# Kernel optimization log

Hardware: AMD Instinct MI355X
Metric: run time of the kernel (lower is better)

The kernel has to match this reference:

```python
import jax, jax.numpy as jnp
import numpy as np
import math

D_MODEL = 1024
NUM_HEADS = 16
HEAD_DIM = D_MODEL // NUM_HEADS
THETA = 10000.0
B, S = 2, 2048


def apply_rope(x, pos, theta=THETA):
    # x: [..., S, D]; pos: [S] int. Rotates consecutive (even, odd) pairs.
    d = x.shape[-1]
    inv_freq = theta ** (-jnp.arange(0, d, 2, dtype=jnp.float32) / d)  # [d/2]
    ang = pos.astype(jnp.float32)[:, None] * inv_freq[None, :]          # [S, d/2]
    cos, sin = jnp.cos(ang), jnp.sin(ang)
    xe = x[..., 0::2]
    xo = x[..., 1::2]
    re = xe * cos - xo * sin
    ro = xe * sin + xo * cos
    return jnp.stack([re, ro], axis=-1).reshape(x.shape)


def setup_inputs() -> dict:
    key = jax.random.key(0)
    ks = jax.random.split(key, 5)
    scale = 1.0 / math.sqrt(D_MODEL)
    return {
        "in_features": jax.random.normal(ks[0], (B, S, D_MODEL), dtype=jnp.float32),
        "token_positions": jnp.arange(S, dtype=jnp.int32),
        "wq": jax.random.normal(ks[1], (D_MODEL, D_MODEL), dtype=jnp.float32) * scale,
        "wk": jax.random.normal(ks[2], (D_MODEL, D_MODEL), dtype=jnp.float32) * scale,
        "wv": jax.random.normal(ks[3], (D_MODEL, D_MODEL), dtype=jnp.float32) * scale,
        "wo": jax.random.normal(ks[4], (D_MODEL, D_MODEL), dtype=jnp.float32) * scale,
    }


def reference(in_features, token_positions, wq, wk, wv, wo):
    x = in_features
    b, s, d = x.shape
    # Linear: y = x @ W.T  (weight stored as [out, in])
    def split_heads(y):
        return y.reshape(b, s, NUM_HEADS, HEAD_DIM).transpose(0, 2, 1, 3)  # [B,H,S,Dh]
    Q = split_heads(x @ wq.T)
    K = split_heads(x @ wk.T)
    V = split_heads(x @ wv.T)
    Q = apply_rope(Q, token_positions)
    K = apply_rope(K, token_positions)
    scores = jnp.einsum('bhqd,bhkd->bhqk', Q, K) / math.sqrt(HEAD_DIM)
    causal = jnp.tril(jnp.ones((s, s), dtype=bool))
    scores = jnp.where(causal, scores, -jnp.inf)
    weights = jax.nn.softmax(scores, axis=-1)
    out = jnp.einsum('bhqk,bhkd->bhqd', weights, V)  # [B,H,S,Dh]
    out = out.transpose(0, 2, 1, 3).reshape(b, s, d)
    return out @ wo.T
```

## Files before the change

kernel.cpp:

```cpp
#include <hip/hip_runtime.h>
#include <hip/hip_bf16.h>

typedef __bf16 bf16_t;
typedef __bf16 bf16x8 __attribute__((ext_vector_type(8)));
typedef __bf16 bf16x4 __attribute__((ext_vector_type(4)));
typedef float  f32x4  __attribute__((ext_vector_type(4)));
typedef float  f32x16 __attribute__((ext_vector_type(16)));
typedef unsigned int u32;
typedef unsigned int u32x2v __attribute__((ext_vector_type(2)));
typedef unsigned int u32x4v __attribute__((ext_vector_type(4)));

#define D_MODEL   1024
#define NQKV      3072
#define NUM_HEADS 16
#define HEAD_DIM  64
#define SEQ       2048
#define BATCH     2
#define NTOK      4096
#define SM_SCALE_LOG2E 0.18033688011112042f
#define NEG_BIG  (-3.0e38f)

__device__ __forceinline__ int swz128(int row, int bytecol) {
  return row*128 + ((((bytecol>>4) ^ (row&7))<<4) | (bytecol & 15));
}

__device__ __forceinline__ void gload16(const void* g, void* l) {
  __builtin_amdgcn_global_load_lds((const __attribute__((address_space(1))) u32*)g,
                                   (__attribute__((address_space(3))) u32*)l, 16, 0, 0);
}

__device__ __forceinline__ u32 cvtpk_bf16(float a, float b) {
  u32 r;
  asm("v_cvt_pk_bf16_f32 %0, %1, %2" : "=v"(r) : "v"(a), "v"(b));
  return r;
}

__device__ __forceinline__ void plswap(u32 &a, u32 &b) {
#if __has_builtin(__builtin_amdgcn_permlane32_swap)
  u32x2v r = __builtin_amdgcn_permlane32_swap(a, b, false, false);
  a = r[0]; b = r[1];
#else
  u32 xa = __shfl_xor((unsigned)a, 32, 64);
  u32 xb = __shfl_xor((unsigned)b, 32, 64);
  bool hi = (threadIdx.x & 32) != 0;
  a = hi ? xb : a;
  b = hi ? b : xa;
#endif
}

__device__ const unsigned char slot_order96[96] = {
  30,31,88,90,92,93,94,95,
  28,29,80,82,84,85,86,87,89,91,
  26,27,72,74,76,77,78,79,81,83,
  24,25,64,66,68,69,70,71,73,75,
  22,23,56,58,60,61,62,63,65,67,
  20,21,48,50,52,53,54,55,57,59,
  18,19,40,42,44,45,46,47,49,51,
  16,17,32,34,36,37,38,39,41,43,
  14,15,33,35,
  12,13, 10,11, 8,9, 6,7, 4,5, 2,3, 0,1
};

__global__ void cvt_x(const float* __restrict__ in, bf16_t* __restrict__ out) {
  int i = (blockIdx.x*256 + threadIdx.x)*4;
  float4 v = *reinterpret_cast<const float4*>(in + i);
  bf16x4 o; o[0]=(bf16_t)v.x; o[1]=(bf16_t)v.y; o[2]=(bf16_t)v.z; o[3]=(bf16_t)v.w;
  *reinterpret_cast<bf16x4*>(out + i) = o;
}

__global__ void cvt_w(const float* __restrict__ wq, const float* __restrict__ wk,
                      const float* __restrict__ wv, const float* __restrict__ wo,
                      bf16_t* __restrict__ wqkv, bf16_t* __restrict__ wob) {
  const int NW = D_MODEL*D_MODEL;
  int i = (blockIdx.x*256 + threadIdx.x)*4;
  float4 v;
  if      (i <   NW) v = *reinterpret_cast<const float4*>(wq + i);
  else if (i < 2*NW) v = *reinterpret_cast<const float4*>(wk + i - NW);
  else if (i < 3*NW) v = *reinterpret_cast<const float4*>(wv + i - 2*NW);
  else               v = *reinterpret_cast<const float4*>(wo + i - 3*NW);
  bf16x4 o; o[0]=(bf16_t)v.x; o[1]=(bf16_t)v.y; o[2]=(bf16_t)v.z; o[3]=(bf16_t)v.w;
  bf16_t* dst = (i < 3*NW) ? (wqkv + i) : (wob + i - 3*NW);
  *reinterpret_cast<bf16x4*>(dst) = o;
}

__global__ void rope_qk(bf16_t* __restrict__ QKV, const int* __restrict__ pos) {
  int i = blockIdx.x*256 + threadIdx.x;
  int j = i & 31;
  int hp = (i >> 5) & 15;
  int t  = i >> 9;
  float ang = (float)pos[t & (SEQ-1)] * exp2f(-(float)j * (13.287712379549449f/32.0f));
  float sv, cv; sincosf(ang, &sv, &cv);
  size_t base = (size_t)t*NQKV + hp*64 + 2*j;
  float xe = (float)QKV[base], xo = (float)QKV[base+1];
  QKV[base]   = (bf16_t)((xe*cv - xo*sv)*SM_SCALE_LOG2E);
  QKV[base+1] = (bf16_t)((xe*sv + xo*cv)*SM_SCALE_LOG2E);
  xe = (float)QKV[base+1024]; xo = (float)QKV[base+1025];
  QKV[base+1024] = (bf16_t)(xe*cv - xo*sv);
  QKV[base+1025] = (bf16_t)(xe*sv + xo*cv);
}

template<typename OutT, bool QKV>
__global__ __launch_bounds__(256, 1) void gemm8(const bf16_t* __restrict__ A,
                                                const bf16_t* __restrict__ B,
                                                OutT* __restrict__ C,
                                                bf16_t* __restrict__ Vt,
                                                int M, int N, int K) {
  __shared__ __align__(16) char lds[4][32768];
  int tid = threadIdx.x;
  int n0 = blockIdx.x*128, m0 = blockIdx.y*128;
  int wid = tid>>6, lane = tid&63;
  int wr = wid>>1, wc = wid&1;
  int lr = lane&15, lg = lane>>4;

  const int nT = K >> 6;

  int srow = tid >> 3;
  int sc8  = (tid & 7) ^ (srow & 7);
  const bf16_t* ga = A + (size_t)(m0 + srow)*K + sc8*8;
  const bf16_t* gb = B + (size_t)(n0 + srow)*K + sc8*8;

  f32x4 acc[4][4];
  #pragma unroll
  for (int a=0;a<4;a++)
    #pragma unroll
    for (int b=0;b<4;b++) acc[a][b] = (f32x4){0.f,0.f,0.f,0.f};

  auto stage = [&](int t) {
    char* s = lds[t&3];
    int k0 = t << 6;
    #pragma unroll
    for (int g=0; g<4; g++)
      gload16(ga + (size_t)(g*32)*K + k0, s + g*4096 + tid*16);
    #pragma unroll
    for (int g=0; g<4; g++)
      gload16(gb + (size_t)(g*32)*K + k0, s + 16384 + g*4096 + tid*16);
  };

  stage(0);
  if (nT > 1) stage(1);
  asm volatile("s_waitcnt vmcnt(8)" ::: "memory");
  __builtin_amdgcn_sched_barrier(0);
  __builtin_amdgcn_s_barrier();

  for (int t = 0; t < nT; ++t) {
    char* sA = lds[t&3];
    char* sB = sA + 16384;

    bf16x8 bq[4][2], aq[2][2];
    #pragma unroll
    for (int ni=0; ni<4; ni++)
      #pragma unroll
      for (int ks=0; ks<2; ks++)
        bq[ni][ks] = *reinterpret_cast<const bf16x8*>(sB + swz128(wc*64+ni*16+lr, ks*64+lg*16));
    #pragma unroll
    for (int mi=0; mi<2; mi++)
      #pragma unroll
      for (int ks=0; ks<2; ks++)
        aq[mi][ks] = *reinterpret_cast<const bf16x8*>(sA + swz128(wr*64+mi*16+lr, ks*64+lg*16));
    if (t + 2 < nT) stage(t + 2);
    asm volatile("s_waitcnt lgkmcnt(0)" ::: "memory");
    __builtin_amdgcn_sched_barrier(0);
    __builtin_amdgcn_s_setprio(1);
    #pragma unroll
    for (int mi=0; mi<2; mi++)
      #pragma unroll
      for (int ni=0; ni<4; ni++)
        #pragma unroll
        for (int ks=0; ks<2; ks++)
          acc[mi][ni] = __builtin_amdgcn_mfma_f32_16x16x32_bf16(aq[mi][ks], bq[ni][ks], acc[mi][ni], 0, 0, 0);
    __builtin_amdgcn_s_setprio(0);
    __builtin_amdgcn_s_barrier();

    bf16x8 aq2[2][2];
    #pragma unroll
    for (int mi=0; mi<2; mi++)
      #pragma unroll
      for (int ks=0; ks<2; ks++)
        aq2[mi][ks] = *reinterpret_cast<const bf16x8*>(sA + swz128(wr*64+(mi+2)*16+lr, ks*64+lg*16));
    asm volatile("s_waitcnt lgkmcnt(0)" ::: "memory");
    __builtin_amdgcn_sched_barrier(0);
    __builtin_amdgcn_s_setprio(1);
    #pragma unroll
    for (int mi=0; mi<2; mi++)
      #pragma unroll
      for (int ni=0; ni<4; ni++)
        #pragma unroll
        for (int ks=0; ks<2; ks++)
          acc[mi+2][ni] = __builtin_amdgcn_mfma_f32_16x16x32_bf16(aq2[mi][ks], bq[ni][ks], acc[mi+2][ni], 0, 0, 0);
    __builtin_amdgcn_s_setprio(0);
    if (t + 2 < nT)      { asm volatile("s_waitcnt vmcnt(8)" ::: "memory"); }
    else if (t + 1 < nT) { asm volatile("s_waitcnt vmcnt(0)" ::: "memory"); }
    __builtin_amdgcn_sched_barrier(0);
    __builtin_amdgcn_s_barrier();
  }

  if (!QKV || n0 < 2*D_MODEL) {
    #pragma unroll
    for (int mi=0;mi<4;mi++)
      #pragma unroll
      for (int ni=0;ni<4;ni++)
        #pragma unroll
        for (int r=0;r<4;r++) {
          int m = m0 + wr*64 + mi*16 + lg*4 + r;
          int n = n0 + wc*64 + ni*16 + lr;
          C[(size_t)m*N + n] = (OutT)acc[mi][ni][r];
        }
  } else {
    #pragma unroll
    for (int mi=0;mi<4;mi++)
      #pragma unroll
      for (int ni=0;ni<4;ni++)
        #pragma unroll
        for (int r=0;r<4;r++) {
          int m = m0 + wr*64 + mi*16 + lg*4 + r;
          int nl = n0 + wc*64 + ni*16 + lr - 2*D_MODEL;
          int h = nl >> 6, d = nl & 63;
          int bb = m >> 11, s = m & (SEQ-1);
          Vt[(((size_t)(bb*16 + h)*64 + d) << 11) + s] = (bf16_t)acc[mi][ni][r];
        }
  }
}

__global__ __launch_bounds__(64, 2) void attn9(const bf16_t* __restrict__ QKV,
                                               const bf16_t* __restrict__ Vt,
                                               bf16_t* __restrict__ pO,
                                               float2* __restrict__ pML) {
  __shared__ __align__(16) char sK[64*128];
  __shared__ __align__(16) char sV[64*128];

  int bh = blockIdx.x;
  int b = bh >> 4, h = bh & 15;
  int lane = threadIdx.x & 63;
  int q32 = lane & 31, hi = lane >> 5;
  int rsub = lane >> 3, sg = (lane & 7) ^ rsub;

  int s = slot_order96[blockIdx.y];
  int qw, t0, t1;
  if (s < 32) { qw = s; t0 = 0; t1 = (s >> 1) + 1; }
  else {
    int e = s - 32;
    qw = 32 + (e >> 1);
    int nt = (qw >> 1) + 1, h0 = (nt + 1) >> 1;
    t0 = (e & 1) ? h0 : 0;
    t1 = (e & 1) ? nt : h0;
  }
  int qt   = qw >> 1;
  int slot = bh*96 + s;
  int qg   = qw*32 + q32;

  bf16x8 qf[4];
  const bf16_t* qrow = QKV + (size_t)(b*SEQ + qw*32 + q32)*NQKV + h*64 + hi*8;
  #pragma unroll
  for (int d=0; d<4; d++) qf[d] = *reinterpret_cast<const bf16x8*>(qrow + d*16);

  const bf16_t* kgb = QKV + D_MODEL + ((size_t)(b*SEQ) + rsub)*NQKV + h*64 + sg*8;
  const bf16_t* vgb = Vt + (size_t)bh*64*SEQ + (size_t)rsub*SEQ + sg*8;

  auto stageK = [&](int t) {
    const bf16_t* src = kgb + (size_t)t*64*NQKV;
    #pragma unroll
    for (int c=0;c<8;c++)
      gload16(src + (size_t)(8*c)*NQKV, sK + c*1024 + lane*16);
  };
  auto stageV = [&](int t) {
    const bf16_t* src = vgb + t*64;
    #pragma unroll
    for (int c=0;c<8;c++)
      gload16(src + (size_t)(8*c)*SEQ, sV + c*1024 + lane*16);
  };

  f32x16 O0 = (f32x16)0.0f, O1 = (f32x16)0.0f;
  float mrun = NEG_BIG, lrun = 0.f;

  stageK(t0); stageV(t0);
  asm volatile("s_waitcnt vmcnt(0)" ::: "memory");
  __builtin_amdgcn_sched_barrier(0);

  for (int ti = t0; ti < t1; ++ti) {
    bf16x8 k0f[4], k1f[4], v0f[4], v1f[4];
    #pragma unroll
    for (int ds=0; ds<4; ds++) {
      k0f[ds] = *reinterpret_cast<const bf16x8*>(sK + swz128(q32,    ds*32 + hi*16));
      k1f[ds] = *reinterpret_cast<const bf16x8*>(sK + swz128(32+q32, ds*32 + hi*16));
      v0f[ds] = *reinterpret_cast<const bf16x8*>(sV + swz128(q32,    ds*32 + hi*16));
      v1f[ds] = *reinterpret_cast<const bf16x8*>(sV + swz128(32+q32, ds*32 + hi*16));
    }
    asm volatile("s_waitcnt lgkmcnt(0)" ::: "memory");
    __builtin_amdgcn_sched_barrier(0);
    if (ti + 1 < t1) { stageK(ti + 1); stageV(ti + 1); }

    f32x16 p0 = (f32x16)0.0f, p1 = (f32x16)0.0f;
    __builtin_amdgcn_s_setprio(1);
    #pragma unroll
    for (int ds=0; ds<4; ds++) {
      p0 = __builtin_amdgcn_mfma_f32_32x32x16_bf16(k0f[ds], qf[ds], p0, 0, 0, 0);
      p1 = __builtin_amdgcn_mfma_f32_32x32x16_bf16(k1f[ds], qf[ds], p1, 0, 0, 0);
    }
    __builtin_amdgcn_s_setprio(0);

    if (ti == qt) {
      #pragma unroll
      for (int r=0; r<16; r++) {
        int kg = ti*64 + (r&3) + 8*(r>>2) + 4*hi;
        if (kg      > qg) p0[r] = NEG_BIG;
        if (kg + 32 > qg) p1[r] = NEG_BIG;
      }
    }

    float mx[8];
    #pragma unroll
    for (int r=0;r<8;r++) mx[r] = fmaxf(fmaxf(p0[r],p0[r+8]), fmaxf(p1[r],p1[r+8]));
    #pragma unroll
    for (int st=4; st>0; st>>=1)
      #pragma unroll
      for (int r=0;r<st;r++) mx[r] = fmaxf(mx[r], mx[r+st]);
    float mt   = fmaxf(mx[0], __shfl_xor(mx[0], 32, 64));
    float mnew = fmaxf(mrun, mt);
    float alpha = exp2f(mrun - mnew);
    #pragma unroll
    for (int r=0; r<16; r++) {
      p0[r] = exp2f(p0[r] - mnew);
      p1[r] = exp2f(p1[r] - mnew);
    }
    float sx[8];
    #pragma unroll
    for (int r=0;r<8;r++) sx[r] = (p0[r]+p0[r+8]) + (p1[r]+p1[r+8]);
    #pragma unroll
    for (int st=4; st>0; st>>=1)
      #pragma unroll
      for (int r=0;r<st;r++) sx[r] += sx[r+st];
    float stot = sx[0] + __shfl_xor(sx[0], 32, 64);
    lrun = lrun*alpha + stot;
    mrun = mnew;
    O0 *= alpha; O1 *= alpha;

    u32 pk0[8], pk1[8];
    #pragma unroll
    for (int i2=0; i2<8; i2++) {
      pk0[i2] = cvtpk_bf16(p0[2*i2], p0[2*i2+1]);
      pk1[i2] = cvtpk_bf16(p1[2*i2], p1[2*i2+1]);
    }
    plswap(pk0[0], pk0[2]); plswap(pk0[1], pk0[3]);
    plswap(pk0[4], pk0[6]); plswap(pk0[5], pk0[7]);
    plswap(pk1[0], pk1[2]); plswap(pk1[1], pk1[3]);
    plswap(pk1[4], pk1[6]); plswap(pk1[5], pk1[7]);

    bf16x8 pa[4];
    pa[0] = __builtin_bit_cast(bf16x8, (u32x4v){pk0[0],pk0[1],pk0[2],pk0[3]});
    pa[1] = __builtin_bit_cast(bf16x8, (u32x4v){pk0[4],pk0[5],pk0[6],pk0[7]});
    pa[2] = __builtin_bit_cast(bf16x8, (u32x4v){pk1[0],pk1[1],pk1[2],pk1[3]});
    pa[3] = __builtin_bit_cast(bf16x8, (u32x4v){pk1[4],pk1[5],pk1[6],pk1[7]});

    __builtin_amdgcn_s_setprio(1);
    #pragma unroll
    for (int ks=0; ks<4; ks++) {
      O0 = __builtin_amdgcn_mfma_f32_32x32x16_bf16(v0f[ks], pa[ks], O0, 0, 0, 0);
      O1 = __builtin_amdgcn_mfma_f32_32x32x16_bf16(v1f[ks], pa[ks], O1, 0, 0, 0);
    }
    __builtin_amdgcn_s_setprio(0);

    if (ti + 1 < t1) {
      asm volatile("s_waitcnt vmcnt(0)" ::: "memory");
      __builtin_amdgcn_sched_barrier(0);
    }
  }

  bf16_t* prow = pO + ((size_t)slot*2048 + q32*64);
  #pragma unroll
  for (int rg=0; rg<4; rg++) {
    int d0 = 8*rg + 4*hi;
    u32 a0 = cvtpk_bf16(O0[4*rg],   O0[4*rg+1]);
    u32 a1 = cvtpk_bf16(O0[4*rg+2], O0[4*rg+3]);
    *reinterpret_cast<u32x2v*>(prow + d0) = (u32x2v){a0, a1};
    u32 b0 = cvtpk_bf16(O1[4*rg],   O1[4*rg+1]);
    u32 b1 = cvtpk_bf16(O1[4*rg+2], O1[4*rg+3]);
    *reinterpret_cast<u32x2v*>(prow + 32 + d0) = (u32x2v){b0, b1};
  }
  if (hi == 0)
    pML[slot*32 + q32] = make_float2(mrun, lrun);
}

__global__ __launch_bounds__(128) void combine(const bf16_t* __restrict__ pO,
                                               const float2* __restrict__ pML,
                                               bf16_t* __restrict__ Of) {
  int qw = blockIdx.x, bh = blockIdx.y;
  int b = bh >> 4, h = bh & 15;
  int t = threadIdx.x;
  int q = t >> 2, d0 = (t & 3) * 16;
  bf16x8 r0, r1;
  if (qw < 32) {
    int slot = bh*96 + qw;
    float2 ml = pML[slot*32 + q];
    float inv = 1.0f / ml.y;
    const bf16x8* src = reinterpret_cast<const bf16x8*>(pO + (size_t)slot*2048 + q*64 + d0);
    bf16x8 o0 = src[0], o1 = src[1];
    #pragma unroll
    for (int i=0;i<8;i++) {
      r0[i] = (bf16_t)((float)o0[i]*inv);
      r1[i] = (bf16_t)((float)o1[i]*inv);
    }
  } else {
    int s0 = bh*96 + 32 + (qw-32)*2;
    float2 mlA = pML[s0*32 + q];
    float2 mlB = pML[(s0+1)*32 + q];
    float m  = fmaxf(mlA.x, mlB.x);
    float a0 = exp2f(mlA.x - m), a1 = exp2f(mlB.x - m);
    float inv = 1.0f / (a0*mlA.y + a1*mlB.y);
    a0 *= inv; a1 *= inv;
    const bf16x8* sA = reinterpret_cast<const bf16x8*>(pO + (size_t)s0*2048 + q*64 + d0);
    const bf16x8* sB = reinterpret_cast<const bf16x8*>(pO + (size_t)(s0+1)*2048 + q*64 + d0);
    bf16x8 oa0 = sA[0], oa1 = sA[1], ob0 = sB[0], ob1 = sB[1];
    #pragma unroll
    for (int i=0;i<8;i++) {
      r0[i] = (bf16_t)(a0*(float)oa0[i] + a1*(float)ob0[i]);
      r1[i] = (bf16_t)(a0*(float)oa1[i] + a1*(float)ob1[i]);
    }
  }
  bf16x8* dst = reinterpret_cast<bf16x8*>(Of + ((size_t)(b*SEQ) + qw*32 + q)*D_MODEL + h*64 + d0);
  dst[0] = r0; dst[1] = r1;
}

extern "C" void kernel_launch(void* const* d_in, const int* in_sizes, int n_in,
                              void* d_out, int out_size, void* d_ws, size_t ws_size,
                              hipStream_t stream) {
  const float* x   = (const float*)d_in[0];
  const int*   pos = (const int*)  d_in[1];
  const float* wq  = (const float*)d_in[2];
  const float* wk  = (const float*)d_in[3];
  const float* wv  = (const float*)d_in[4];
  const float* wo  = (const float*)d_in[5];
  float* out = (float*)d_out;

  char* ws = (char*)d_ws;
  bf16_t* xb   = (bf16_t*)(ws);
  bf16_t* wqkv = (bf16_t*)(ws + ( 8u<<20));
  bf16_t* wob  = (bf16_t*)(ws + (14u<<20));
  bf16_t* QKV  = (bf16_t*)(ws + (16u<<20));
  bf16_t* Vtb  = (bf16_t*)(ws + (40u<<20));
  bf16_t* pO   = (bf16_t*)(ws);
  float2* pML  = (float2*)(ws + (13u<<20));
  bf16_t* Of   = (bf16_t*)(ws + (40u<<20));

  cvt_x<<<NTOK*D_MODEL/1024, 256, 0, stream>>>(x, xb);
  cvt_w<<<4*D_MODEL*D_MODEL/1024, 256, 0, stream>>>(wq, wk, wv, wo, wqkv, wob);

  dim3 gqkv(NQKV/128, NTOK/128);
  gemm8<bf16_t, true><<<gqkv, 256, 0, stream>>>(xb, wqkv, QKV, Vtb, NTOK, NQKV, D_MODEL);

  rope_qk<<<NTOK*NUM_HEADS*32/256, 256, 0, stream>>>(QKV, pos);

  dim3 gattn(32, 96);
  attn9<<<gattn, 64, 0, stream>>>(QKV, Vtb, pO, pML);

  dim3 gcomb(64, 32);
  combine<<<gcomb, 128, 0, stream>>>(pO, pML, Of);

  dim3 gout(D_MODEL/128, NTOK/128);
  gemm8<float, false><<<gout, 256, 0, stream>>>(Of, wob, out, nullptr, NTOK, D_MODEL, D_MODEL);
}
```

Before: 131.3 us.

## Load V fragments directly from global, add lazy softmax rescale, raise occupancy

The attention kernel stops staging the transposed V tile through shared memory and reads V fragments straight from global memory into registers. This halves LDS use per block, and launch bounds rise from 2 to 3 waves per SIMD. The online softmax now rescales only when some lane's row max grows by more than 8 (in log2 units) over the running max, which skips the exp and multiply of the O accumulators on most tiles. The trade-off is that V global loads are no longer prefetched a tile ahead, so their latency is exposed. Raising the launch bound may also limit registers enough to cause spills.

```diff
diff --git a/kernel.cpp b/kernel.cpp
--- a/kernel.cpp
+++ b/kernel.cpp
@@ -221,12 +221,11 @@
   }
 }
 
-__global__ __launch_bounds__(64, 2) void attn9(const bf16_t* __restrict__ QKV,
-                                               const bf16_t* __restrict__ Vt,
-                                               bf16_t* __restrict__ pO,
-                                               float2* __restrict__ pML) {
+__global__ __launch_bounds__(64, 3) void attn10(const bf16_t* __restrict__ QKV,
+                                                const bf16_t* __restrict__ Vt,
+                                                bf16_t* __restrict__ pO,
+                                                float2* __restrict__ pML) {
   __shared__ __align__(16) char sK[64*128];
-  __shared__ __align__(16) char sV[64*128];
 
   int bh = blockIdx.x;
   int b = bh >> 4, h = bh & 15;
@@ -254,7 +253,8 @@
   for (int d=0; d<4; d++) qf[d] = *reinterpret_cast<const bf16x8*>(qrow + d*16);
 
   const bf16_t* kgb = QKV + D_MODEL + ((size_t)(b*SEQ) + rsub)*NQKV + h*64 + sg*8;
-  const bf16_t* vgb = Vt + (size_t)bh*64*SEQ + (size_t)rsub*SEQ + sg*8;
+  const bf16_t* vg0 = Vt + (size_t)bh*64*SEQ + (size_t)q32*SEQ + hi*8;
+  const bf16_t* vg1 = vg0 + (size_t)32*SEQ;
 
   auto stageK = [&](int t) {
     const bf16_t* src = kgb + (size_t)t*64*NQKV;
@@ -262,32 +262,30 @@
     for (int c=0;c<8;c++)
       gload16(src + (size_t)(8*c)*NQKV, sK + c*1024 + lane*16);
   };
-  auto stageV = [&](int t) {
-    const bf16_t* src = vgb + t*64;
-    #pragma unroll
-    for (int c=0;c<8;c++)
-      gload16(src + (size_t)(8*c)*SEQ, sV + c*1024 + lane*16);
-  };
 
   f32x16 O0 = (f32x16)0.0f, O1 = (f32x16)0.0f;
   float mrun = NEG_BIG, lrun = 0.f;
 
-  stageK(t0); stageV(t0);
+  stageK(t0);
   asm volatile("s_waitcnt vmcnt(0)" ::: "memory");
   __builtin_amdgcn_sched_barrier(0);
 
   for (int ti = t0; ti < t1; ++ti) {
-    bf16x8 k0f[4], k1f[4], v0f[4], v1f[4];
+    bf16x8 k0f[4], k1f[4];
     #pragma unroll
     for (int ds=0; ds<4; ds++) {
       k0f[ds] = *reinterpret_cast<const bf16x8*>(sK + swz128(q32,    ds*32 + hi*16));
       k1f[ds] = *reinterpret_cast<const bf16x8*>(sK + swz128(32+q32, ds*32 + hi*16));
-      v0f[ds] = *reinterpret_cast<const bf16x8*>(sV + swz128(q32,    ds*32 + hi*16));
-      v1f[ds] = *reinterpret_cast<const bf16x8*>(sV + swz128(32+q32, ds*32 + hi*16));
+    }
+    bf16x8 v0f[4], v1f[4];
+    #pragma unroll
+    for (int ks=0; ks<4; ks++) {
+      v0f[ks] = *reinterpret_cast<const bf16x8*>(vg0 + ti*64 + ks*16);
+      v1f[ks] = *reinterpret_cast<const bf16x8*>(vg1 + ti*64 + ks*16);
     }
     asm volatile("s_waitcnt lgkmcnt(0)" ::: "memory");
     __builtin_amdgcn_sched_barrier(0);
-    if (ti + 1 < t1) { stageK(ti + 1); stageV(ti + 1); }
+    if (ti + 1 < t1) stageK(ti + 1);
 
     f32x16 p0 = (f32x16)0.0f, p1 = (f32x16)0.0f;
     __builtin_amdgcn_s_setprio(1);
@@ -314,13 +312,19 @@
     for (int st=4; st>0; st>>=1)
       #pragma unroll
       for (int r=0;r<st;r++) mx[r] = fmaxf(mx[r], mx[r+st]);
-    float mt   = fmaxf(mx[0], __shfl_xor(mx[0], 32, 64));
-    float mnew = fmaxf(mrun, mt);
-    float alpha = exp2f(mrun - mnew);
+    float mt = fmaxf(mx[0], __shfl_xor(mx[0], 32, 64));
+
+    if (!__all(mt <= mrun + 8.0f)) {
+      float mnew  = fmaxf(mrun, mt);
+      float alpha = exp2f(mrun - mnew);
+      lrun *= alpha;
+      O0 *= alpha; O1 *= alpha;
+      mrun = mnew;
+    }
     #pragma unroll
     for (int r=0; r<16; r++) {
-      p0[r] = exp2f(p0[r] - mnew);
-      p1[r] = exp2f(p1[r] - mnew);
+      p0[r] = exp2f(p0[r] - mrun);
+      p1[r] = exp2f(p1[r] - mrun);
     }
     float sx[8];
     #pragma unroll
@@ -329,10 +333,7 @@
     for (int st=4; st>0; st>>=1)
       #pragma unroll
       for (int r=0;r<st;r++) sx[r] += sx[r+st];
-    float stot = sx[0] + __shfl_xor(sx[0], 32, 64);
-    lrun = lrun*alpha + stot;
-    mrun = mnew;
-    O0 *= alpha; O1 *= alpha;
+    lrun += sx[0] + __shfl_xor(sx[0], 32, 64);
 
     u32 pk0[8], pk1[8];
     #pragma unroll
@@ -450,7 +451,7 @@
   rope_qk<<<NTOK*NUM_HEADS*32/256, 256, 0, stream>>>(QKV, pos);
 
   dim3 gattn(32, 96);
-  attn9<<<gattn, 64, 0, stream>>>(QKV, Vtb, pO, pML);
+  attn10<<<gattn, 64, 0, stream>>>(QKV, Vtb, pO, pML);
 
   dim3 gcomb(64, 32);
   combine<<<gcomb, 128, 0, stream>>>(pO, pML, Of);
```

Result: slower. 136.9 us (+4.3%).

## Fuse RoPE into QKV GEMM epilogue and merge conversion kernels

Applied to the files above, without the earlier changes.

Removes the standalone rope_qk kernel by applying rotary embedding and the Q softmax scale inside the QKV GEMM epilogue. Adjacent even/odd columns are paired with a lane shuffle, and the angle comes from a fast __sincosf. The separate x and weight fp32-to-bf16 conversion kernels are also merged into one launch. This removes a read-modify-write pass over Q/K and a kernel launch, at the cost of more epilogue work and lower sin/cos accuracy at large angles.

```diff
diff --git a/kernel.cpp b/kernel.cpp
--- a/kernel.cpp
+++ b/kernel.cpp
@@ -18,6 +18,7 @@
 #define BATCH     2
 #define NTOK      4096
 #define SM_SCALE_LOG2E 0.18033688011112042f
+#define LOG2_THETA 13.287712379549449f
 #define NEG_BIG  (-3.0e38f)
 
 __device__ __forceinline__ int swz128(int row, int bytecol) {
@@ -61,42 +62,25 @@
   12,13, 10,11, 8,9, 6,7, 4,5, 2,3, 0,1
 };
 
-__global__ void cvt_x(const float* __restrict__ in, bf16_t* __restrict__ out) {
-  int i = (blockIdx.x*256 + threadIdx.x)*4;
-  float4 v = *reinterpret_cast<const float4*>(in + i);
-  bf16x4 o; o[0]=(bf16_t)v.x; o[1]=(bf16_t)v.y; o[2]=(bf16_t)v.z; o[3]=(bf16_t)v.w;
-  *reinterpret_cast<bf16x4*>(out + i) = o;
-}
-
-__global__ void cvt_w(const float* __restrict__ wq, const float* __restrict__ wk,
-                      const float* __restrict__ wv, const float* __restrict__ wo,
-                      bf16_t* __restrict__ wqkv, bf16_t* __restrict__ wob) {
+__global__ void cvt_all(const float* __restrict__ x,  const float* __restrict__ wq,
+                        const float* __restrict__ wk, const float* __restrict__ wv,
+                        const float* __restrict__ wo,
+                        bf16_t* __restrict__ xb, bf16_t* __restrict__ wqkv,
+                        bf16_t* __restrict__ wob) {
+  const int NX = NTOK*D_MODEL;
   const int NW = D_MODEL*D_MODEL;
   int i = (blockIdx.x*256 + threadIdx.x)*4;
-  float4 v;
-  if      (i <   NW) v = *reinterpret_cast<const float4*>(wq + i);
-  else if (i < 2*NW) v = *reinterpret_cast<const float4*>(wk + i - NW);
-  else if (i < 3*NW) v = *reinterpret_cast<const float4*>(wv + i - 2*NW);
-  else               v = *reinterpret_cast<const float4*>(wo + i - 3*NW);
+  float4 v; bf16_t* dst;
+  if (i < NX) { v = *reinterpret_cast<const float4*>(x + i); dst = xb + i; }
+  else {
+    int k = i - NX;
+    if      (k <   NW) { v = *reinterpret_cast<const float4*>(wq + k);        dst = wqkv + k; }
+    else if (k < 2*NW) { v = *reinterpret_cast<const float4*>(wk + k -   NW); dst = wqkv + k; }
+    else if (k < 3*NW) { v = *reinterpret_cast<const float4*>(wv + k - 2*NW); dst = wqkv + k; }
+    else               { v = *reinterpret_cast<const float4*>(wo + k - 3*NW); dst = wob + k - 3*NW; }
+  }
   bf16x4 o; o[0]=(bf16_t)v.x; o[1]=(bf16_t)v.y; o[2]=(bf16_t)v.z; o[3]=(bf16_t)v.w;
-  bf16_t* dst = (i < 3*NW) ? (wqkv + i) : (wob + i - 3*NW);
   *reinterpret_cast<bf16x4*>(dst) = o;
-}
-
-__global__ void rope_qk(bf16_t* __restrict__ QKV, const int* __restrict__ pos) {
-  int i = blockIdx.x*256 + threadIdx.x;
-  int j = i & 31;
-  int hp = (i >> 5) & 15;
-  int t  = i >> 9;
-  float ang = (float)pos[t & (SEQ-1)] * exp2f(-(float)j * (13.287712379549449f/32.0f));
-  float sv, cv; sincosf(ang, &sv, &cv);
-  size_t base = (size_t)t*NQKV + hp*64 + 2*j;
-  float xe = (float)QKV[base], xo = (float)QKV[base+1];
-  QKV[base]   = (bf16_t)((xe*cv - xo*sv)*SM_SCALE_LOG2E);
-  QKV[base+1] = (bf16_t)((xe*sv + xo*cv)*SM_SCALE_LOG2E);
-  xe = (float)QKV[base+1024]; xo = (float)QKV[base+1025];
-  QKV[base+1024] = (bf16_t)(xe*cv - xo*sv);
-  QKV[base+1025] = (bf16_t)(xe*sv + xo*cv);
 }
 
 template<typename OutT, bool QKV>
@@ -104,6 +88,7 @@
                                                 const bf16_t* __restrict__ B,
                                                 OutT* __restrict__ C,
                                                 bf16_t* __restrict__ Vt,
+                                                const int* __restrict__ pos,
                                                 int M, int N, int K) {
   __shared__ __align__(16) char lds[4][32768];
   int tid = threadIdx.x;
@@ -194,7 +179,33 @@
     __builtin_amdgcn_s_barrier();
   }
 
-  if (!QKV || n0 < 2*D_MODEL) {
+  if (QKV && n0 < 2*D_MODEL) {
+    bool isQ = (n0 < D_MODEL);
+    float fr[4];
+    #pragma unroll
+    for (int ni=0; ni<4; ni++) {
+      int j = ((wc*64 + ni*16 + lr) & 63) >> 1;
+      fr[ni] = exp2f(-(float)j * (LOG2_THETA/32.0f));
+    }
+    #pragma unroll
+    for (int mi=0; mi<4; mi++)
+      #pragma unroll
+      for (int r=0; r<4; r++) {
+        int m = m0 + wr*64 + mi*16 + lg*4 + r;
+        float pt = (float)pos[m & (SEQ-1)];
+        #pragma unroll
+        for (int ni=0; ni<4; ni++) {
+          int n = n0 + wc*64 + ni*16 + lr;
+          float v = acc[mi][ni][r];
+          float p = __shfl_xor(v, 1, 64);
+          float sv, cv;
+          __sincosf(pt * fr[ni], &sv, &cv);
+          float o = (n & 1) ? (p*sv + v*cv) : (v*cv - p*sv);
+          if (isQ) o *= SM_SCALE_LOG2E;
+          C[(size_t)m*N + n] = (OutT)o;
+        }
+      }
+  } else if (!QKV) {
     #pragma unroll
     for (int mi=0;mi<4;mi++)
       #pragma unroll
@@ -441,13 +452,10 @@
   float2* pML  = (float2*)(ws + (13u<<20));
   bf16_t* Of   = (bf16_t*)(ws + (40u<<20));
 
-  cvt_x<<<NTOK*D_MODEL/1024, 256, 0, stream>>>(x, xb);
-  cvt_w<<<4*D_MODEL*D_MODEL/1024, 256, 0, stream>>>(wq, wk, wv, wo, wqkv, wob);
+  cvt_all<<<8*D_MODEL*D_MODEL/1024, 256, 0, stream>>>(x, wq, wk, wv, wo, xb, wqkv, wob);
 
   dim3 gqkv(NQKV/128, NTOK/128);
-  gemm8<bf16_t, true><<<gqkv, 256, 0, stream>>>(xb, wqkv, QKV, Vtb, NTOK, NQKV, D_MODEL);
-
-  rope_qk<<<NTOK*NUM_HEADS*32/256, 256, 0, stream>>>(QKV, pos);
+  gemm8<bf16_t, true><<<gqkv, 256, 0, stream>>>(xb, wqkv, QKV, Vtb, pos, NTOK, NQKV, D_MODEL);
 
   dim3 gattn(32, 96);
   attn9<<<gattn, 64, 0, stream>>>(QKV, Vtb, pO, pML);
@@ -456,5 +464,5 @@
   combine<<<gcomb, 128, 0, stream>>>(pO, pML, Of);
 
   dim3 gout(D_MODEL/128, NTOK/128);
-  gemm8<float, false><<<gout, 256, 0, stream>>>(Of, wob, out, nullptr, NTOK, D_MODEL, D_MODEL);
-}
+  gemm8<float, false><<<gout, 256, 0, stream>>>(Of, wob, out, nullptr, nullptr, NTOK, D_MODEL, D_MODEL);
+}
```

Result: faster. 125.5 us (-4.4%).
